# Performance work log

Measured on AMD Instinct MI355X. Metric: run time of the kernel, lower is better.

Reference implementation:

```python
import jax, jax.numpy as jnp
import numpy as np

D, H, HD, DEPTH, V, L, BOS = 128, 16, 8, 16, 17, 1024, 16

def _ln(x, s, b):
    m = jnp.mean(x, -1, keepdims=True)
    v = jnp.mean((x - m) ** 2, -1, keepdims=True)
    return (x - m) * jax.lax.rsqrt(v + 1e-5) * s + b

def _transformer(tok, emb, pos, layers, lnf_s, lnf_b, head_w, head_b):
    # tok: [B,S] int tokens. GPT-style pre-LN decoder, causal attention.
    B, S = tok.shape
    h = emb[tok] + pos[:S]
    causal = jnp.tril(jnp.ones((S, S), dtype=bool))
    inv_sqrt = np.float32(1.0 / np.sqrt(HD))
    def layer(h, p):
        ln1_s, ln1_b, wqkv, bqkv, wo, bo, ln2_s, ln2_b, w1, b1, w2, b2 = p
        x = _ln(h, ln1_s, ln1_b)
        qkv = x @ wqkv + bqkv  # [B,S,3D]
        q, k, v = jnp.split(qkv, 3, axis=-1)
        q = q.reshape(B, S, H, HD)
        k = k.reshape(B, S, H, HD)
        v = v.reshape(B, S, H, HD)
        att = jnp.einsum('bshd,bthd->bhst', q, k) * inv_sqrt
        att = jax.nn.softmax(jnp.where(causal, att, -1e9), axis=-1)
        o = jnp.einsum('bhst,bthd->bshd', att, v).reshape(B, S, D)
        h = h + o @ wo + bo
        x = _ln(h, ln2_s, ln2_b)
        h = h + jax.nn.gelu(x @ w1 + b1) @ w2 + b2
        return h, None
    h, _ = jax.lax.scan(layer, h, layers)
    return _ln(h, lnf_s, lnf_b) @ head_w + head_b  # [B,S,V]

def setup_inputs() -> dict:
    key = jax.random.key(0)
    ks = jax.random.split(key, 8)
    s = 0.02
    return {
        'tokens': jax.random.randint(ks[0], (1, L), 0, BOS, dtype=jnp.int32),
        'emb': jax.random.normal(ks[1], (V, D), jnp.float32) * s,
        'pos': jax.random.normal(ks[2], (L, D), jnp.float32) * s,
        'ln1_s': jnp.ones((DEPTH, D)), 'ln1_b': jnp.zeros((DEPTH, D)),
        'wqkv': jax.random.normal(ks[3], (DEPTH, D, 3 * D), jnp.float32) * s,
        'bqkv': jnp.zeros((DEPTH, 3 * D)),
        'wo': jax.random.normal(ks[4], (DEPTH, D, D), jnp.float32) * s,
        'bo': jnp.zeros((DEPTH, D)),
        'ln2_s': jnp.ones((DEPTH, D)), 'ln2_b': jnp.zeros((DEPTH, D)),
        'w1': jax.random.normal(ks[5], (DEPTH, D, 4 * D), jnp.float32) * s,
        'b1': jnp.zeros((DEPTH, 4 * D)),
        'w2': jax.random.normal(ks[6], (DEPTH, 4 * D, D), jnp.float32) * s,
        'b2': jnp.zeros((DEPTH, D)),
        'lnf_s': jnp.ones((D,)), 'lnf_b': jnp.zeros((D,)),
        'head_w': jax.random.normal(ks[7], (D, V), jnp.float32) * s,
        'head_b': jnp.zeros((V,)),
    }

def reference(tokens, emb, pos, ln1_s, ln1_b, wqkv, bqkv, wo, bo, ln2_s, ln2_b, w1, b1, w2, b2, lnf_s, lnf_b, head_w, head_b):
    layers = (ln1_s, ln1_b, wqkv, bqkv, wo, bo, ln2_s, ln2_b, w1, b1, w2, b2)
    tf = lambda t: _transformer(t, emb, pos, layers, lnf_s, lnf_b, head_w, head_b)
    # BOS-pad (pad value == num_embeddings == 16), as in F.pad(latent,(1,0),value=16)
    lat = jnp.concatenate([jnp.full((1, 1), BOS, jnp.int32), tokens.astype(jnp.int32)], axis=1)  # [1,1025]
    # likelihood pass: next-token log-prob of each latent token
    logits = tf(lat[:, :L])                               # [1,1024,V]
    logp = jax.nn.log_softmax(logits, axis=-1)
    ll = jnp.take_along_axis(logp, lat[:, 1:, None], axis=-1)[..., 0]  # [1,1024]
    mask = ll[0] < jnp.quantile(ll, 0.03)
    # token-healing loop: per masked position, rerun transformer, argmax (BOS excluded)
    def body(i, lat):
        def heal(lat):
            lg = tf(lat[:, :L])  # causal => position i-1 equals prefix-run logits
            row = jax.lax.dynamic_index_in_dim(lg, i - 1, axis=1, keepdims=False)[0]  # [V]
            probs = jax.nn.softmax(row).at[BOS].set(0.0)
            return lat.at[:, i].set(jnp.argmax(probs).astype(jnp.int32))
        return jax.lax.cond(mask[i - 1], heal, lambda l: l, lat)
    lat = jax.lax.fori_loop(1, L + 1, body, lat)
    out_logits = tf(lat[:, :L])  # logits over healed sequence (float output)
    return (out_logits, lat[:, 1:])
```

## Files before the change

### kernel.cpp

```cpp
#include <hip/hip_runtime.h>
#include <math.h>

#define D 128
#define NLAYER 16
#define V 17
#define L 1024
#define BOSX 16
#define NWG 256
#define NT 512

struct P {
  const int* tokens;
  const float *emb, *pos, *ln1_s, *ln1_b, *wqkv, *bqkv, *wo, *bo;
  const float *ln2_s, *ln2_b, *w1, *b1, *w2, *b2, *lnf_s, *lnf_b, *hw, *hb;
  float *kc, *vc, *ll_;
  int *lat, *heal_row, *barc, *done, *heals_done, *prog;
  float *logits, *out_tok;
};

__device__ __forceinline__ void stUf(float* p, float v) {
  __hip_atomic_store(p, v, __ATOMIC_RELAXED, __HIP_MEMORY_SCOPE_SYSTEM);
}
__device__ __forceinline__ int ldUi(const int* p) {
  return __hip_atomic_load((int*)p, __ATOMIC_RELAXED, __HIP_MEMORY_SCOPE_SYSTEM);
}
__device__ __forceinline__ void stUi(int* p, int v) {
  __hip_atomic_store(p, v, __ATOMIC_RELAXED, __HIP_MEMORY_SCOPE_SYSTEM);
}

__device__ __forceinline__ void barFull(int* cnt, int& b) {
  asm volatile("s_waitcnt vmcnt(0)" ::: "memory");
  __syncthreads();
  if (threadIdx.x == 0) {
    __threadfence();
    __hip_atomic_fetch_add(cnt, 1, __ATOMIC_RELAXED, __HIP_MEMORY_SCOPE_AGENT);
    int tgt = (b + 1) * NWG;
    while (__hip_atomic_load(cnt, __ATOMIC_RELAXED, __HIP_MEMORY_SCOPE_AGENT) < tgt)
      __builtin_amdgcn_s_sleep(8);
    __threadfence();
  }
  b += 1;
  __syncthreads();
}

__device__ __forceinline__ float geluf(float a) {
  float cgv = 0.7978845608028654f * (a + 0.044715f * a * a * a);
  cgv = fminf(fmaxf(cgv, -15.f), 15.f);
  float e = __expf(2.f * cgv);
  return 0.5f * a * (1.f + (e - 1.f) / (e + 1.f));
}

__device__ void lnorm(const float* __restrict__ s, const float* __restrict__ b,
                      const float* in, float* out, float* red) {
  int t = threadIdx.x;
  float v = (t < D) ? in[t] : 0.f;
  float sm = v;
#pragma unroll
  for (int o = 32; o; o >>= 1) sm += __shfl_xor(sm, o, 64);
  if (t < D && (t & 63) == 0) red[t >> 6] = sm;
  __syncthreads();
  float mean = (red[0] + red[1]) * (1.f / 128.f);
  float d = (t < D) ? (v - mean) : 0.f;
  float vs = d * d;
#pragma unroll
  for (int o = 32; o; o >>= 1) vs += __shfl_xor(vs, o, 64);
  if (t < D && (t & 63) == 0) red[2 + (t >> 6)] = vs;
  __syncthreads();
  float rstd = rsqrtf((red[2] + red[3]) * (1.f / 128.f) + 1e-5f);
  if (t < D) out[t] = d * rstd * s[t] + b[t];
  __syncthreads();
}

template <bool HEAL>
__device__ void qkvPub(const P& p, int l, int row, int split, const float* x, float* qrow) {
  int t = threadIdx.x;
  if (t < 384) {
    const float* w = p.wqkv + (size_t)l * D * 384 + t;
    float a = 0.f;
#pragma unroll 16
    for (int d = 0; d < D; ++d) a += x[d] * w[d * 384];
    a += p.bqkv[l * 384 + t];
    float* kcl = p.kc + (size_t)l * L * D + (size_t)row * D;
    float* vcl = p.vc + (size_t)l * L * D + (size_t)row * D;
    if (t < 128) qrow[t] = a;
    else if (t < 256) { if (HEAL) stUf(&kcl[t - 128], a); else kcl[t - 128] = a; }
    else              { if (HEAL) stUf(&vcl[t - 256], a); else vcl[t - 256] = a; }
  }
  if (HEAL) {
    asm volatile("s_waitcnt vmcnt(0)" ::: "memory");
    __syncthreads();
    if (t == 0) {
      int* dl = p.done + l * L;
      if (row - 1 >= split)
        while (ldUi(&dl[row - 1]) < 1) __builtin_amdgcn_s_sleep(1);
      stUi(&dl[row], 1);
    }
    __syncthreads();
  } else {
    __syncthreads();
  }
}

__device__ void attnProjFFN(const P& p, int row, int l,
                            float* hrow, const float* qrow,
                            float* oS, float* xnS, float* fS, float* padS, float* redS) {
  int t = threadIdx.x;
  const float* kcl = p.kc + (size_t)l * L * D;
  const float* vcl = p.vc + (size_t)l * L * D;
  int head = t >> 5, lane = t & 31;
  const float* qh = qrow + head * 8;
  float q0=qh[0],q1=qh[1],q2=qh[2],q3=qh[3],q4=qh[4],q5=qh[5],q6=qh[6],q7=qh[7];
  float sum = 0.f, a0=0,a1=0,a2=0,a3=0,a4=0,a5=0,a6=0,a7=0;
#pragma unroll 2
  for (int key = lane; key <= row; key += 32) {
    const float4* kp = (const float4*)(kcl + (size_t)key * D + head * 8);
    float4 k0 = kp[0], k1 = kp[1];
    float sc = q0*k0.x+q1*k0.y+q2*k0.z+q3*k0.w+q4*k1.x+q5*k1.y+q6*k1.z+q7*k1.w;
    float pr = __expf(sc * 0.35355339059327376f);
    const float4* vp = (const float4*)(vcl + (size_t)key * D + head * 8);
    float4 v0 = vp[0], v1 = vp[1];
    sum += pr;
    a0+=pr*v0.x; a1+=pr*v0.y; a2+=pr*v0.z; a3+=pr*v0.w;
    a4+=pr*v1.x; a5+=pr*v1.y; a6+=pr*v1.z; a7+=pr*v1.w;
  }
#pragma unroll
  for (int o = 1; o < 32; o <<= 1) {
    sum += __shfl_xor(sum, o, 32);
    a0 += __shfl_xor(a0, o, 32); a1 += __shfl_xor(a1, o, 32);
    a2 += __shfl_xor(a2, o, 32); a3 += __shfl_xor(a3, o, 32);
    a4 += __shfl_xor(a4, o, 32); a5 += __shfl_xor(a5, o, 32);
    a6 += __shfl_xor(a6, o, 32); a7 += __shfl_xor(a7, o, 32);
  }
  if (lane == 0) {
    float inv = 1.f / sum;
    oS[head*8+0]=a0*inv; oS[head*8+1]=a1*inv; oS[head*8+2]=a2*inv; oS[head*8+3]=a3*inv;
    oS[head*8+4]=a4*inv; oS[head*8+5]=a5*inv; oS[head*8+6]=a6*inv; oS[head*8+7]=a7*inv;
  }
  __syncthreads();
  {
    int col = t & 127, seg = t >> 7;
    const float* wp = p.wo + (size_t)l * D * D + col;
    float acc = 0.f;
    int d0 = seg * 32;
#pragma unroll 8
    for (int d = d0; d < d0 + 32; ++d) acc += oS[d] * wp[d * D];
    padS[t] = acc;
  }
  __syncthreads();
  if (t < D) hrow[t] += padS[t] + padS[t+128] + padS[t+256] + padS[t+384] + p.bo[l * D + t];
  __syncthreads();
  lnorm(p.ln2_s + l * D, p.ln2_b + l * D, hrow, xnS, redS);
  {
    const float* w1p = p.w1 + (size_t)l * D * 512 + t;
    float acc = 0.f;
#pragma unroll 16
    for (int d = 0; d < D; ++d) acc += xnS[d] * w1p[d * 512];
    fS[t] = geluf(acc + p.b1[l * 512 + t]);
  }
  __syncthreads();
  {
    int col = t & 127, seg = t >> 7;
    const float* w2p = p.w2 + (size_t)l * 512 * D + col;
    float acc = 0.f;
    int d0 = seg * 128;
#pragma unroll 16
    for (int d = d0; d < d0 + 128; ++d) acc += fS[d] * w2p[d * D];
    padS[t] = acc;
  }
  __syncthreads();
  if (t < D) hrow[t] += padS[t] + padS[t+128] + padS[t+256] + padS[t+384] + p.b2[l * D + t];
  __syncthreads();
}

template <bool HEAL>
__device__ void headRow(const P& p, int row, float* hrow,
                        float* xnS, float* redS, float* padS, float* oS) {
  lnorm(p.lnf_s, p.lnf_b, hrow, xnS, redS);
  int t = threadIdx.x;
  if (t < V * 8) {
    int col = t >> 3, seg = t & 7;
    float acc = 0.f;
    int d0 = seg * 16;
#pragma unroll
    for (int d = d0; d < d0 + 16; ++d) acc += xnS[d] * p.hw[d * V + col];
    padS[t] = acc;
  }
  __syncthreads();
  if (t < V) {
    float a = padS[t*8]+padS[t*8+1]+padS[t*8+2]+padS[t*8+3]
            + padS[t*8+4]+padS[t*8+5]+padS[t*8+6]+padS[t*8+7] + p.hb[t];
    oS[t] = a;
    if (HEAL) stUf(&p.logits[row * V + t], a);
    else      p.logits[row * V + t] = a;
  }
  __syncthreads();
}

__global__ void kInit(const int* __restrict__ tokens, int* __restrict__ lat,
                      int* __restrict__ barc, int* __restrict__ done,
                      int* __restrict__ hd) {
  int i = blockIdx.x * blockDim.x + threadIdx.x;
  if (i == 0) stUi(lat, BOSX);
  if (i < L) stUi(lat + i + 1, tokens[i]);
  if (i < 64) stUi(barc + i, 0);
  if (i < 16) stUi(hd + i, 0);
  if (i < NLAYER * L) stUi(done + i, 0);
}

__global__ void __launch_bounds__(NT, 1) kMega(P p) {
  __shared__ float hS[4][D];
  __shared__ float qS[4][D];
  __shared__ float xnS[D];
  __shared__ float oS[D];
  __shared__ float fS[512];
  __shared__ float padS[512];
  __shared__ float redS[16];
  __shared__ float sortS[L];
  __shared__ int cntS[NT + 1];
  int wg = blockIdx.x, t = threadIdx.x;
  int b = 0;
  int* cnt = p.barc;

  for (int i = 0; i < 4; ++i) {
    int row = wg + i * NWG;
    int tok = p.lat[row];
    if (t < D) hS[i][t] = p.emb[tok * D + t] + p.pos[row * D + t];
    __syncthreads();
    lnorm(p.ln1_s, p.ln1_b, hS[i], xnS, redS);
    qkvPub<false>(p, 0, row, 0, xnS, qS[i]);
  }
  barFull(cnt, b);
  for (int l = 0; l < NLAYER; ++l) {
    for (int i = 0; i < 4; ++i) {
      int row = wg + i * NWG;
      attnProjFFN(p, row, l, hS[i], qS[i], oS, xnS, fS, padS, redS);
      if (l < NLAYER - 1) {
        lnorm(p.ln1_s + (l+1)*D, p.ln1_b + (l+1)*D, hS[i], xnS, redS);
        qkvPub<false>(p, l + 1, row, 0, xnS, qS[i]);
      } else {
        headRow<false>(p, row, hS[i], xnS, redS, padS, oS);
      }
    }
    barFull(cnt, b);
  }

  {
    int gid = wg * NT + t;
    if (gid < L) {
      float r[V];
#pragma unroll
      for (int v = 0; v < V; ++v) r[v] = p.logits[gid * V + v];
      float m = r[0];
#pragma unroll
      for (int v = 1; v < V; ++v) m = fmaxf(m, r[v]);
      float s = 0.f;
#pragma unroll
      for (int v = 0; v < V; ++v) s += expf(r[v] - m);
      p.ll_[gid] = r[p.lat[gid + 1]] - (m + logf(s));
    }
  }
  barFull(cnt, b);

  if (wg == 0) {
    for (int i = t; i < L; i += NT) sortS[i] = p.ll_[i];
    __syncthreads();
    for (int ksz = 2; ksz <= L; ksz <<= 1) {
      for (int j = ksz >> 1; j; j >>= 1) {
        for (int i = t; i < L; i += NT) {
          int l2 = i ^ j;
          if (l2 > i) {
            bool up = ((i & ksz) == 0);
            float a = sortS[i], bb = sortS[l2];
            if ((a > bb) == up) { sortS[i] = bb; sortS[l2] = a; }
          }
        }
        __syncthreads();
      }
    }
    if (t == 0) {
      double frac = 0.03 * 1023.0 - 30.0;
      redS[0] = (float)((double)sortS[30] + frac * ((double)sortS[31] - (double)sortS[30]));
    }
    __syncthreads();
    float val = redS[0];
    float lv0 = p.ll_[t * 2], lv1 = p.ll_[t * 2 + 1];
    int loc[2], cc = 0;
    if (lv0 < val) loc[cc++] = t * 2;
    if (lv1 < val) loc[cc++] = t * 2 + 1;
    cntS[t] = cc;
    __syncthreads();
    if (t == 0) {
      int run = 0;
      for (int i = 0; i < NT; ++i) { int c2 = cntS[i]; cntS[i] = run; run += c2; }
      cntS[NT] = run;
    }
    __syncthreads();
    int base = cntS[t];
    for (int j = 0; j < cc; ++j)
      if (base + j < 31) p.heal_row[base + j] = loc[j];
    __syncthreads();
    if (t == 0) {
      int c = cntS[NT]; if (c > 31) c = 31;
      p.heal_row[31] = c;
      stUi(p.heals_done, 1);
      if (c > 0) {
        int r0 = p.heal_row[0];
        int best = 0; float bv = p.logits[r0 * V];
        for (int v = 1; v < BOSX; ++v) {
          float x = p.logits[r0 * V + v];
          if (x > bv) { bv = x; best = v; }
        }
        stUi(&p.lat[r0 + 1], best);
      }
    }
  }
  barFull(cnt, b);

  int c = p.heal_row[31];
  int split = (c > 0) ? (p.heal_row[0] + 1) : L;
  for (int r = split + wg; r < L; r += NWG) {
    int nh = 0, hk = -1;
    bool leadRow = false;
    for (int j = 0; j < c; ++j) {
      nh += (p.heal_row[j] < r) ? 1 : 0;
      if (j >= 1 && p.heal_row[j] == r) hk = j;
      if (p.heal_row[j] == r - 1) leadRow = true;
    }
    {
      int pfi = (wg * 11) % 224;
      for (;;) {
        if (t == 0) { cntS[0] = ldUi(p.heals_done); cntS[1] = ldUi(p.prog); }
        __syncthreads();
        int hd = cntS[0];
        int pl = (cntS[1] + 1) & 15;
        if (hd >= nh) break;
        int dist = nh - hd;
        if (leadRow && dist == 1) {
          __builtin_amdgcn_s_sleep(1);
          __syncthreads();
          continue;
        }
        int R = p.heal_row[hd - 1];
        float sink = 0.f;
#pragma unroll
        for (int j2 = 0; j2 < 6; ++j2) {
          int ch = pfi + j2; if (ch >= 224) ch -= 224;
          const float* basep = nullptr;
          if (ch < 24)      basep = p.wqkv + (size_t)pl * D * 384 + ch * 2048;
          else if (ch < 32) basep = p.wo   + (size_t)pl * D * D   + (ch - 24) * 2048;
          else if (ch < 64) basep = p.w1   + (size_t)pl * D * 512 + (ch - 32) * 2048;
          else if (ch < 96) basep = p.w2   + (size_t)pl * 512 * D + (ch - 64) * 2048;
          else {
            int kvch = ch - 96;
            int blk = (kvch & 63) * 16;
            if (blk + 15 <= R)
              basep = (kvch < 64 ? p.kc : p.vc) + (size_t)pl * L * D + (size_t)blk * D;
          }
          if (basep) {
            float4 v = *(const float4*)(basep + t * 4);
            sink += v.x + v.y + v.z + v.w;
          }
        }
        asm volatile("" :: "v"(sink));
        pfi += 6; if (pfi >= 224) pfi -= 224;
        if (dist >= 4) {
          __builtin_amdgcn_s_sleep(127); __builtin_amdgcn_s_sleep(127);
          __builtin_amdgcn_s_sleep(127); __builtin_amdgcn_s_sleep(127);
        } else if (dist >= 2) {
          __builtin_amdgcn_s_sleep(127);
        } else {
          __builtin_amdgcn_s_sleep(32);
        }
        __syncthreads();
      }
      if (t == 0) cntS[0] = ldUi(&p.lat[r]);
      __syncthreads();
    }
    int tok = cntS[0];
    if (t < D) hS[0][t] = p.emb[tok * D + t] + p.pos[r * D + t];
    __syncthreads();
    lnorm(p.ln1_s, p.ln1_b, hS[0], xnS, redS);
    qkvPub<true>(p, 0, r, split, xnS, qS[0]);
    for (int l = 0; l < NLAYER; ++l) {
      if (leadRow && t == 0) stUi(p.prog, l);
      attnProjFFN(p, r, l, hS[0], qS[0], oS, xnS, fS, padS, redS);
      if (l < NLAYER - 1) {
        lnorm(p.ln1_s + (l+1)*D, p.ln1_b + (l+1)*D, hS[0], xnS, redS);
        qkvPub<true>(p, l + 1, r, split, xnS, qS[0]);
      } else {
        headRow<true>(p, r, hS[0], xnS, redS, padS, oS);
      }
    }
    if (hk >= 0 && t == 0) {
      int best = 0; float bv = oS[0];
      for (int v = 1; v < BOSX; ++v)
        if (oS[v] > bv) { bv = oS[v]; best = v; }
      stUi(&p.lat[r + 1], best);
      asm volatile("s_waitcnt vmcnt(0)" ::: "memory");
      stUi(p.heals_done, hk + 1);
    }
  }

  barFull(cnt, b);

  {
    int gid = wg * NT + t;
    if (gid < L) p.out_tok[gid] = (float)ldUi(&p.lat[gid + 1]);
  }
}

extern "C" void kernel_launch(void* const* d_in, const int* in_sizes, int n_in,
                              void* d_out, int out_size, void* d_ws, size_t ws_size,
                              hipStream_t stream) {
  P prm;
  prm.tokens = (const int*)d_in[0];
  prm.emb    = (const float*)d_in[1];
  prm.pos    = (const float*)d_in[2];
  prm.ln1_s  = (const float*)d_in[3];
  prm.ln1_b  = (const float*)d_in[4];
  prm.wqkv   = (const float*)d_in[5];
  prm.bqkv   = (const float*)d_in[6];
  prm.wo     = (const float*)d_in[7];
  prm.bo     = (const float*)d_in[8];
  prm.ln2_s  = (const float*)d_in[9];
  prm.ln2_b  = (const float*)d_in[10];
  prm.w1     = (const float*)d_in[11];
  prm.b1     = (const float*)d_in[12];
  prm.w2     = (const float*)d_in[13];
  prm.b2     = (const float*)d_in[14];
  prm.lnf_s  = (const float*)d_in[15];
  prm.lnf_b  = (const float*)d_in[16];
  prm.hw     = (const float*)d_in[17];
  prm.hb     = (const float*)d_in[18];

  float* ws = (float*)d_ws;
  prm.kc   = ws;
  prm.vc   = prm.kc + (size_t)NLAYER*L*D;
  prm.ll_  = prm.vc + (size_t)NLAYER*L*D;
  prm.lat        = (int*)(prm.ll_ + L);
  prm.heal_row   = prm.lat + 1032;
  prm.barc       = prm.heal_row + 32;
  prm.done       = prm.barc + 64;
  prm.heals_done = prm.done + NLAYER * L;
  prm.prog       = prm.heals_done + 8;

  prm.logits  = (float*)d_out;
  prm.out_tok = prm.logits + L * V;

  kInit<<<64, 256, 0, stream>>>(prm.tokens, prm.lat, prm.barc, prm.done, prm.heals_done);

  void* args[] = { &prm };
  (void)hipLaunchCooperativeKernel((const void*)kMega, dim3(NWG), dim3(NT), args, 0, stream);
}
```

Before: 17.42 ms.

## Double workgroup size to 1024 threads and split matvec reductions across halves

Raises the block size from 512 to 1024 threads. The QKV and W1 matvecs now split the reduction dimension into two halves and reduce them through shared memory. The Wo and W2 matvecs use 8 segments instead of 4, and attention gives each head a full 64-lane wavefront. The bitonic sort and mask scan are simplified to one element per thread. The aim is to cut per-row latency in the serial healing chain by using more threads, at the cost of extra syncs, register pressure under launch bounds of 1024, and more shared memory.

```diff
diff --git a/kernel.cpp b/kernel.cpp
--- a/kernel.cpp
+++ b/kernel.cpp
@@ -7,7 +7,7 @@
 #define L 1024
 #define BOSX 16
 #define NWG 256
-#define NT 512
+#define NT 1024
 
 struct P {
   const int* tokens;
@@ -72,14 +72,22 @@
 }
 
 template <bool HEAL>
-__device__ void qkvPub(const P& p, int l, int row, int split, const float* x, float* qrow) {
+__device__ void qkvPub(const P& p, int l, int row, int split, const float* x,
+                       float* qrow, float* padS) {
   int t = threadIdx.x;
+  int half = (t >= 512) ? 1 : 0;
+  int cq = half ? (t - 512) : t;
+  if (cq < 384) {
+    const float* w = p.wqkv + (size_t)l * D * 384 + cq;
+    float a = 0.f;
+    int d0 = half * 64;
+#pragma unroll 16
+    for (int d = d0; d < d0 + 64; ++d) a += x[d] * w[d * 384];
+    padS[half * 384 + cq] = a;
+  }
+  __syncthreads();
   if (t < 384) {
-    const float* w = p.wqkv + (size_t)l * D * 384 + t;
-    float a = 0.f;
-#pragma unroll 16
-    for (int d = 0; d < D; ++d) a += x[d] * w[d * 384];
-    a += p.bqkv[l * 384 + t];
+    float a = padS[t] + padS[384 + t] + p.bqkv[l * 384 + t];
     float* kcl = p.kc + (size_t)l * L * D + (size_t)row * D;
     float* vcl = p.vc + (size_t)l * L * D + (size_t)row * D;
     if (t < 128) qrow[t] = a;
@@ -107,68 +115,87 @@
   int t = threadIdx.x;
   const float* kcl = p.kc + (size_t)l * L * D;
   const float* vcl = p.vc + (size_t)l * L * D;
-  int head = t >> 5, lane = t & 31;
-  const float* qh = qrow + head * 8;
-  float q0=qh[0],q1=qh[1],q2=qh[2],q3=qh[3],q4=qh[4],q5=qh[5],q6=qh[6],q7=qh[7];
-  float sum = 0.f, a0=0,a1=0,a2=0,a3=0,a4=0,a5=0,a6=0,a7=0;
+  {
+    int head = t >> 6, lane = t & 63;
+    const float* qh = qrow + head * 8;
+    float q0=qh[0],q1=qh[1],q2=qh[2],q3=qh[3],q4=qh[4],q5=qh[5],q6=qh[6],q7=qh[7];
+    float sum = 0.f, a0=0,a1=0,a2=0,a3=0,a4=0,a5=0,a6=0,a7=0;
 #pragma unroll 2
-  for (int key = lane; key <= row; key += 32) {
-    const float4* kp = (const float4*)(kcl + (size_t)key * D + head * 8);
-    float4 k0 = kp[0], k1 = kp[1];
-    float sc = q0*k0.x+q1*k0.y+q2*k0.z+q3*k0.w+q4*k1.x+q5*k1.y+q6*k1.z+q7*k1.w;
-    float pr = __expf(sc * 0.35355339059327376f);
-    const float4* vp = (const float4*)(vcl + (size_t)key * D + head * 8);
-    float4 v0 = vp[0], v1 = vp[1];
-    sum += pr;
-    a0+=pr*v0.x; a1+=pr*v0.y; a2+=pr*v0.z; a3+=pr*v0.w;
-    a4+=pr*v1.x; a5+=pr*v1.y; a6+=pr*v1.z; a7+=pr*v1.w;
-  }
-#pragma unroll
-  for (int o = 1; o < 32; o <<= 1) {
-    sum += __shfl_xor(sum, o, 32);
-    a0 += __shfl_xor(a0, o, 32); a1 += __shfl_xor(a1, o, 32);
-    a2 += __shfl_xor(a2, o, 32); a3 += __shfl_xor(a3, o, 32);
-    a4 += __shfl_xor(a4, o, 32); a5 += __shfl_xor(a5, o, 32);
-    a6 += __shfl_xor(a6, o, 32); a7 += __shfl_xor(a7, o, 32);
-  }
-  if (lane == 0) {
-    float inv = 1.f / sum;
-    oS[head*8+0]=a0*inv; oS[head*8+1]=a1*inv; oS[head*8+2]=a2*inv; oS[head*8+3]=a3*inv;
-    oS[head*8+4]=a4*inv; oS[head*8+5]=a5*inv; oS[head*8+6]=a6*inv; oS[head*8+7]=a7*inv;
+    for (int key = lane; key <= row; key += 64) {
+      const float4* kp = (const float4*)(kcl + (size_t)key * D + head * 8);
+      float4 k0 = kp[0], k1 = kp[1];
+      float sc = q0*k0.x+q1*k0.y+q2*k0.z+q3*k0.w+q4*k1.x+q5*k1.y+q6*k1.z+q7*k1.w;
+      float pr = __expf(sc * 0.35355339059327376f);
+      const float4* vp = (const float4*)(vcl + (size_t)key * D + head * 8);
+      float4 v0 = vp[0], v1 = vp[1];
+      sum += pr;
+      a0+=pr*v0.x; a1+=pr*v0.y; a2+=pr*v0.z; a3+=pr*v0.w;
+      a4+=pr*v1.x; a5+=pr*v1.y; a6+=pr*v1.z; a7+=pr*v1.w;
+    }
+#pragma unroll
+    for (int o = 1; o < 64; o <<= 1) {
+      sum += __shfl_xor(sum, o, 64);
+      a0 += __shfl_xor(a0, o, 64); a1 += __shfl_xor(a1, o, 64);
+      a2 += __shfl_xor(a2, o, 64); a3 += __shfl_xor(a3, o, 64);
+      a4 += __shfl_xor(a4, o, 64); a5 += __shfl_xor(a5, o, 64);
+      a6 += __shfl_xor(a6, o, 64); a7 += __shfl_xor(a7, o, 64);
+    }
+    if (lane == 0) {
+      float inv = 1.f / sum;
+      oS[head*8+0]=a0*inv; oS[head*8+1]=a1*inv; oS[head*8+2]=a2*inv; oS[head*8+3]=a3*inv;
+      oS[head*8+4]=a4*inv; oS[head*8+5]=a5*inv; oS[head*8+6]=a6*inv; oS[head*8+7]=a7*inv;
+    }
   }
   __syncthreads();
   {
     int col = t & 127, seg = t >> 7;
     const float* wp = p.wo + (size_t)l * D * D + col;
     float acc = 0.f;
-    int d0 = seg * 32;
-#pragma unroll 8
-    for (int d = d0; d < d0 + 32; ++d) acc += oS[d] * wp[d * D];
-    padS[t] = acc;
-  }
-  __syncthreads();
-  if (t < D) hrow[t] += padS[t] + padS[t+128] + padS[t+256] + padS[t+384] + p.bo[l * D + t];
+    int d0 = seg * 16;
+#pragma unroll 16
+    for (int d = d0; d < d0 + 16; ++d) acc += oS[d] * wp[d * D];
+    padS[seg * 128 + col] = acc;
+  }
+  __syncthreads();
+  if (t < D) {
+    float a = 0.f;
+#pragma unroll
+    for (int s = 0; s < 8; ++s) a += padS[s * 128 + t];
+    hrow[t] += a + p.bo[l * D + t];
+  }
   __syncthreads();
   lnorm(p.ln2_s + l * D, p.ln2_b + l * D, hrow, xnS, redS);
   {
-    const float* w1p = p.w1 + (size_t)l * D * 512 + t;
+    int half = (t >= 512) ? 1 : 0;
+    int cq = half ? (t - 512) : t;
+    const float* w1p = p.w1 + (size_t)l * D * 512 + cq;
     float acc = 0.f;
+    int d0 = half * 64;
 #pragma unroll 16
-    for (int d = 0; d < D; ++d) acc += xnS[d] * w1p[d * 512];
-    fS[t] = geluf(acc + p.b1[l * 512 + t]);
+    for (int d = d0; d < d0 + 64; ++d) acc += xnS[d] * w1p[d * 512];
+    padS[half * 512 + cq] = acc;
+  }
+  __syncthreads();
+  if (t < 512) {
+    fS[t] = geluf(padS[t] + padS[512 + t] + p.b1[l * 512 + t]);
   }
   __syncthreads();
   {
     int col = t & 127, seg = t >> 7;
     const float* w2p = p.w2 + (size_t)l * 512 * D + col;
     float acc = 0.f;
-    int d0 = seg * 128;
+    int d0 = seg * 64;
 #pragma unroll 16
-    for (int d = d0; d < d0 + 128; ++d) acc += fS[d] * w2p[d * D];
-    padS[t] = acc;
-  }
-  __syncthreads();
-  if (t < D) hrow[t] += padS[t] + padS[t+128] + padS[t+256] + padS[t+384] + p.b2[l * D + t];
+    for (int d = d0; d < d0 + 64; ++d) acc += fS[d] * w2p[d * D];
+    padS[seg * 128 + col] = acc;
+  }
+  __syncthreads();
+  if (t < D) {
+    float a = 0.f;
+#pragma unroll
+    for (int s = 0; s < 8; ++s) a += padS[s * 128 + t];
+    hrow[t] += a + p.b2[l * D + t];
+  }
   __syncthreads();
 }
 
@@ -213,7 +240,7 @@
   __shared__ float xnS[D];
   __shared__ float oS[D];
   __shared__ float fS[512];
-  __shared__ float padS[512];
+  __shared__ float padS[1024];
   __shared__ float redS[16];
   __shared__ float sortS[L];
   __shared__ int cntS[NT + 1];
@@ -227,7 +254,7 @@
     if (t < D) hS[i][t] = p.emb[tok * D + t] + p.pos[row * D + t];
     __syncthreads();
     lnorm(p.ln1_s, p.ln1_b, hS[i], xnS, redS);
-    qkvPub<false>(p, 0, row, 0, xnS, qS[i]);
+    qkvPub<false>(p, 0, row, 0, xnS, qS[i], padS);
   }
   barFull(cnt, b);
   for (int l = 0; l < NLAYER; ++l) {
@@ -236,7 +263,7 @@
       attnProjFFN(p, row, l, hS[i], qS[i], oS, xnS, fS, padS, redS);
       if (l < NLAYER - 1) {
         lnorm(p.ln1_s + (l+1)*D, p.ln1_b + (l+1)*D, hS[i], xnS, redS);
-        qkvPub<false>(p, l + 1, row, 0, xnS, qS[i]);
+        qkvPub<false>(p, l + 1, row, 0, xnS, qS[i], padS);
       } else {
         headRow<false>(p, row, hS[i], xnS, redS, padS, oS);
       }
@@ -262,17 +289,15 @@
   barFull(cnt, b);
 
   if (wg == 0) {
-    for (int i = t; i < L; i += NT) sortS[i] = p.ll_[i];
+    sortS[t] = p.ll_[t];
     __syncthreads();
     for (int ksz = 2; ksz <= L; ksz <<= 1) {
       for (int j = ksz >> 1; j; j >>= 1) {
-        for (int i = t; i < L; i += NT) {
-          int l2 = i ^ j;
-          if (l2 > i) {
-            bool up = ((i & ksz) == 0);
-            float a = sortS[i], bb = sortS[l2];
-            if ((a > bb) == up) { sortS[i] = bb; sortS[l2] = a; }
-          }
+        int pr = t ^ j;
+        if (pr > t) {
+          bool up = ((t & ksz) == 0);
+          float a = sortS[t], bb = sortS[pr];
+          if ((a > bb) == up) { sortS[t] = bb; sortS[pr] = a; }
         }
         __syncthreads();
       }
@@ -283,10 +308,7 @@
     }
     __syncthreads();
     float val = redS[0];
-    float lv0 = p.ll_[t * 2], lv1 = p.ll_[t * 2 + 1];
-    int loc[2], cc = 0;
-    if (lv0 < val) loc[cc++] = t * 2;
-    if (lv1 < val) loc[cc++] = t * 2 + 1;
+    int cc = (p.ll_[t] < val) ? 1 : 0;
     cntS[t] = cc;
     __syncthreads();
     if (t == 0) {
@@ -295,9 +317,7 @@
       cntS[NT] = run;
     }
     __syncthreads();
-    int base = cntS[t];
-    for (int j = 0; j < cc; ++j)
-      if (base + j < 31) p.heal_row[base + j] = loc[j];
+    if (cc && cntS[t] < 31) p.heal_row[cntS[t]] = t;
     __syncthreads();
     if (t == 0) {
       int c = cntS[NT]; if (c > 31) c = 31;
@@ -342,23 +362,25 @@
         }
         int R = p.heal_row[hd - 1];
         float sink = 0.f;
-#pragma unroll
-        for (int j2 = 0; j2 < 6; ++j2) {
-          int ch = pfi + j2; if (ch >= 224) ch -= 224;
-          const float* basep = nullptr;
-          if (ch < 24)      basep = p.wqkv + (size_t)pl * D * 384 + ch * 2048;
-          else if (ch < 32) basep = p.wo   + (size_t)pl * D * D   + (ch - 24) * 2048;
-          else if (ch < 64) basep = p.w1   + (size_t)pl * D * 512 + (ch - 32) * 2048;
-          else if (ch < 96) basep = p.w2   + (size_t)pl * 512 * D + (ch - 64) * 2048;
-          else {
-            int kvch = ch - 96;
-            int blk = (kvch & 63) * 16;
-            if (blk + 15 <= R)
-              basep = (kvch < 64 ? p.kc : p.vc) + (size_t)pl * L * D + (size_t)blk * D;
-          }
-          if (basep) {
-            float4 v = *(const float4*)(basep + t * 4);
-            sink += v.x + v.y + v.z + v.w;
+        if (t < 512) {
+#pragma unroll
+          for (int j2 = 0; j2 < 6; ++j2) {
+            int ch = pfi + j2; if (ch >= 224) ch -= 224;
+            const float* basep = nullptr;
+            if (ch < 24)      basep = p.wqkv + (size_t)pl * D * 384 + ch * 2048;
+            else if (ch < 32) basep = p.wo   + (size_t)pl * D * D   + (ch - 24) * 2048;
+            else if (ch < 64) basep = p.w1   + (size_t)pl * D * 512 + (ch - 32) * 2048;
+            else if (ch < 96) basep = p.w2   + (size_t)pl * 512 * D + (ch - 64) * 2048;
+            else {
+              int kvch = ch - 96;
+              int blk = (kvch & 63) * 16;
+              if (blk + 15 <= R)
+                basep = (kvch < 64 ? p.kc : p.vc) + (size_t)pl * L * D + (size_t)blk * D;
+            }
+            if (basep) {
+              float4 v = *(const float4*)(basep + t * 4);
+              sink += v.x + v.y + v.z + v.w;
+            }
           }
         }
         asm volatile("" :: "v"(sink));
@@ -380,13 +402,13 @@
     if (t < D) hS[0][t] = p.emb[tok * D + t] + p.pos[r * D + t];
     __syncthreads();
     lnorm(p.ln1_s, p.ln1_b, hS[0], xnS, redS);
-    qkvPub<true>(p, 0, r, split, xnS, qS[0]);
+    qkvPub<true>(p, 0, r, split, xnS, qS[0], padS);
     for (int l = 0; l < NLAYER; ++l) {
       if (leadRow && t == 0) stUi(p.prog, l);
       attnProjFFN(p, r, l, hS[0], qS[0], oS, xnS, fS, padS, redS);
       if (l < NLAYER - 1) {
         lnorm(p.ln1_s + (l+1)*D, p.ln1_b + (l+1)*D, hS[0], xnS, redS);
-        qkvPub<true>(p, l + 1, r, split, xnS, qS[0]);
+        qkvPub<true>(p, l + 1, r, split, xnS, qS[0], padS);
       } else {
         headRow<true>(p, r, hS[0], xnS, redS, padS, oS);
       }
```

Result: slower. 31.84 ms (+82.8%).
